# Performance work log

Measured on AMD Instinct MI355X. Metric: run time of the kernel, lower is better.

The kernel has to match this reference:

```python
import jax, jax.numpy as jnp
import numpy as np

N_NODES = 50000
N_EDGES = 800000
IN_C = 128
OUT_C = 128
BN_EPS = 1e-5


def setup_inputs() -> dict:
    key = jax.random.key(0)
    k1, k2, k3 = jax.random.split(key, 3)
    x = jax.random.normal(k1, (N_NODES, IN_C), dtype=jnp.float32)
    edge_index = jax.random.randint(k2, (2, N_EDGES), 0, N_NODES, dtype=jnp.int32)
    W = jax.random.normal(k3, (IN_C, OUT_C), dtype=jnp.float32) * (1.0 / np.sqrt(IN_C))
    bias = jnp.zeros((OUT_C,), dtype=jnp.float32)
    gamma = jnp.ones((OUT_C,), dtype=jnp.float32)
    beta = jnp.zeros((OUT_C,), dtype=jnp.float32)
    return {"x": x, "W": W, "bias": bias, "gamma": gamma, "beta": beta,
            "edge_index": edge_index}


def reference(x, W, bias, gamma, beta, edge_index):
    # GCNConv (PyG defaults): add self-loops, symmetric normalization, linear, scatter-add
    n = x.shape[0]
    h = x @ W  # [N, out_c]
    loops = jnp.arange(n, dtype=edge_index.dtype)
    row = jnp.concatenate([edge_index[0], loops])  # source nodes
    col = jnp.concatenate([edge_index[1], loops])  # target nodes
    # degree of targets (with self-loops, so deg >= 1)
    deg = jnp.zeros((n,), dtype=h.dtype).at[col].add(1.0)
    dinv = jax.lax.rsqrt(deg)
    norm = dinv[row] * dinv[col]  # [E+N]
    msg = h[row] * norm[:, None]  # gather + per-edge scale, [E+N, out_c]
    agg = jax.ops.segment_sum(msg, col, num_segments=n) + bias  # scatter-add
    # BatchNorm1d over node dimension (training-mode batch statistics)
    mean = jnp.mean(agg, axis=0)
    var = jnp.var(agg, axis=0)
    y = (agg - mean) * jax.lax.rsqrt(var + BN_EPS) * gamma + beta
    # ReLU; dropout is identity at inference
    return jax.nn.relu(y)
```

## Files before the change

kernel.cpp:

```cpp
#include <hip/hip_runtime.h>

#define N_NODES 50000
#define N_EDGES 800000
#define C 128
#define BN_EPS 1e-5f
#define BSHIFT 7
#define NBUCK ((N_NODES + 127) >> BSHIFT)
#define EPB 2048
#define A_BLOCKS ((N_EDGES + EPB - 1) / EPB)
#define EBUF 2560
#define GEMM_BLOCKS ((N_NODES + 63) / 64)
#define GATHER_BLOCKS 512
#define GATHER_WAVES (GATHER_BLOCKS * 8)

typedef __attribute__((ext_vector_type(8))) short bf16x8;
typedef __attribute__((ext_vector_type(4))) float f32x4;

__device__ __forceinline__ unsigned pack_bf16x2(float a, float b) {
    unsigned ua = __float_as_uint(a);
    ua = (ua + 0x7FFFu + ((ua >> 16) & 1u)) >> 16;
    unsigned ub = __float_as_uint(b);
    ub = (ub + 0x7FFFu + ((ub >> 16) & 1u)) >> 16;
    return ua | (ub << 16);
}

__device__ __forceinline__ unsigned short bf16_1(float a) {
    unsigned u = __float_as_uint(a);
    return (unsigned short)((u + 0x7FFFu + ((u >> 16) & 1u)) >> 16);
}

__device__ __forceinline__ float blo(unsigned u) { return __uint_as_float(u << 16); }
__device__ __forceinline__ float bhi(unsigned u) { return __uint_as_float(u & 0xFFFF0000u); }

__device__ __forceinline__ unsigned pack_f16x2(float a, float b) {
    _Float16 ha = (_Float16)a, hb = (_Float16)b;
    return (unsigned)__builtin_bit_cast(unsigned short, ha) |
           ((unsigned)__builtin_bit_cast(unsigned short, hb) << 16);
}
__device__ __forceinline__ float f16lo(unsigned u) {
    return (float)__builtin_bit_cast(_Float16, (unsigned short)(u & 0xFFFFu));
}
__device__ __forceinline__ float f16hi(unsigned u) {
    return (float)__builtin_bit_cast(_Float16, (unsigned short)(u >> 16));
}

__global__ void __launch_bounds__(256) k_scat(const int* __restrict__ row,
                                              const int* __restrict__ col,
                                              unsigned* __restrict__ bEdges,
                                              int* __restrict__ bOffsT,
                                              const float* __restrict__ W,
                                              unsigned* __restrict__ WTn,
                                              float* __restrict__ sums8) {
    int tid = threadIdx.x, w = blockIdx.x;
    if (w == A_BLOCKS) {
#pragma unroll
        for (int it = 0; it < 32; ++it) {
            int i = tid + (it << 8);
            int j = i & 3, l = (i >> 2) & 63, kt = (i >> 8) & 3, nt = i >> 10;
            int m = l & 15, q = l >> 4;
            int kr = kt * 32 + q * 8 + 2 * j;
            int n = nt * 16 + m;
            WTn[i] = pack_bf16x2(W[kr * C + n], W[(kr + 1) * C + n]);
        }
        for (int i = tid; i < 2048; i += 256) sums8[i] = 0.f;
        return;
    }
    __shared__ int hist[NBUCK];
    __shared__ int wsum[8];
    int lane = tid & 63, wid = tid >> 6;
    for (int i = tid; i < NBUCK; i += 256) hist[i] = 0;
    __syncthreads();
    int e0 = w * EPB;
    int nE = N_EDGES - e0; if (nE > EPB) nE = EPB;
    int myc[8], myr[8];
#pragma unroll
    for (int k = 0; k < 8; ++k) {
        int idx = tid + (k << 8);
        bool ok = idx < nE;
        myc[k] = ok ? col[e0 + idx] : -1;
        myr[k] = ok ? row[e0 + idx] : 0;
        if (ok) atomicAdd(&hist[myc[k] >> BSHIFT], 1);
    }
    __syncthreads();
    int v0 = hist[tid];
    int v1 = (tid + 256 < NBUCK) ? hist[tid + 256] : 0;
    int s0 = v0, s1 = v1;
#pragma unroll
    for (int d = 1; d < 64; d <<= 1) {
        int u0 = __shfl_up(s0, d, 64);
        int u1 = __shfl_up(s1, d, 64);
        if (lane >= d) { s0 += u0; s1 += u1; }
    }
    if (lane == 63) { wsum[wid] = s0; wsum[4 + wid] = s1; }
    __syncthreads();
    int tot0 = wsum[0] + wsum[1] + wsum[2] + wsum[3];
    int p0 = 0, p1 = tot0;
    for (int i = 0; i < wid; ++i) { p0 += wsum[i]; p1 += wsum[4 + i]; }
    int exc0 = p0 + s0 - v0;
    int exc1 = p1 + s1 - v1;
    bOffsT[tid * A_BLOCKS + w] = exc0;
    if (tid + 256 < NBUCK) bOffsT[(tid + 256) * A_BLOCKS + w] = exc1;
    if (tid == 0) bOffsT[NBUCK * A_BLOCKS + w] = nE;
    hist[tid] = exc0;
    if (tid + 256 < NBUCK) hist[tid + 256] = exc1;
    __syncthreads();
#pragma unroll
    for (int k = 0; k < 8; ++k) {
        if (myc[k] >= 0) {
            int b = myc[k] >> BSHIFT;
            int r = atomicAdd(&hist[b], 1);
            bEdges[(size_t)w * EPB + r] = (unsigned)myr[k] | ((unsigned)myc[k] << 16);
        }
    }
}

__global__ void __launch_bounds__(256) k_mid(const unsigned* __restrict__ bEdges,
                                             const int* __restrict__ bOffsT,
                                             int* __restrict__ offs,
                                             float* __restrict__ dinvArr,
                                             unsigned short* __restrict__ srcs,
                                             const float* __restrict__ x,
                                             const unsigned* __restrict__ WTn,
                                             unsigned short* __restrict__ g16) {
    __shared__ __align__(16) unsigned sm[4352];
    __shared__ int wsum[12];
    __shared__ int wtot;
    int tid = threadIdx.x;
    int lane = tid & 63, wid = tid >> 6;
    if (blockIdx.x < NBUCK) {
        const int b = blockIdx.x;
        int* sS = (int*)sm;
        int* sO = (int*)sm + 392;
        unsigned* ebuf = sm + 792;
        int* h = (int*)(sm + 792 + EBUF);
        int i1 = tid + 256;
        int st0 = bOffsT[b * A_BLOCKS + tid];
        int v0 = bOffsT[(b + 1) * A_BLOCKS + tid] - st0;
        int st1 = 0, v1 = 0;
        if (i1 < A_BLOCKS) {
            st1 = bOffsT[b * A_BLOCKS + i1];
            v1 = bOffsT[(b + 1) * A_BLOCKS + i1] - st1;
        }
        sS[tid] = st0;
        if (i1 < A_BLOCKS) sS[i1] = st1;
        if (tid < 128) h[tid] = 0;
        int ep = st0 + st1;
        int s0 = v0, s1 = v1;
#pragma unroll
        for (int d = 1; d < 64; d <<= 1) {
            int u0 = __shfl_up(s0, d, 64);
            int u1 = __shfl_up(s1, d, 64);
            if (lane >= d) { s0 += u0; s1 += u1; }
            ep += __shfl_xor(ep, d, 64);
        }
        if (lane == 63) { wsum[wid] = s0; wsum[4 + wid] = s1; }
        if (lane == 0) wsum[8 + wid] = ep;
        __syncthreads();
        int tot0 = wsum[0] + wsum[1] + wsum[2] + wsum[3];
        int tot1 = wsum[4] + wsum[5] + wsum[6] + wsum[7];
        int e0 = wsum[8] + wsum[9] + wsum[10] + wsum[11];
        int p0 = 0, p1 = tot0;
        for (int i = 0; i < wid; ++i) { p0 += wsum[i]; p1 += wsum[4 + i]; }
        sO[tid] = p0 + s0 - v0;
        if (i1 < A_BLOCKS) sO[i1] = p1 + s1 - v1;
        if (tid == 0) sO[A_BLOCKS] = tot0 + tot1;
        __syncthreads();
        int c = sO[A_BLOCKS];
        if (c > EBUF) c = EBUF;
        for (int seg = tid; seg < A_BLOCKS; seg += 256) {
            int o = sO[seg];
            int n = sO[seg + 1] - o;
            const unsigned* srcp = bEdges + (size_t)seg * EPB + sS[seg];
            for (int k = 0; k < n; ++k) {
                int dp = o + k;
                if (dp < EBUF) ebuf[dp] = srcp[k];
            }
        }
        __syncthreads();
        int n0 = b << BSHIFT;
        int nn = N_NODES - n0; if (nn > 128) nn = 128;
        for (int e = tid; e < c; e += 256)
            atomicAdd(&h[(int)(ebuf[e] >> 16) - n0], 1);
        __syncthreads();
        int v = 0, sc = 0;
        if (tid < 128) {
            int ln = tid & 63;
            v = h[tid];
            sc = v;
#pragma unroll
            for (int d = 1; d < 64; d <<= 1) {
                int u = __shfl_up(sc, d, 64);
                if (ln >= d) sc += u;
            }
            if (tid == 63) wtot = sc;
        }
        __syncthreads();
        if (tid < 128) {
            int ex = sc - v + ((tid >= 64) ? wtot : 0);
            if (tid < nn) {
                offs[n0 + tid] = e0 + ex;
                dinvArr[n0 + tid] = rsqrtf((float)v + 1.f);
            }
            h[tid] = ex;
        }
        __syncthreads();
        for (int e = tid; e < c; e += 256) {
            unsigned pe = ebuf[e];
            int r = atomicAdd(&h[(int)(pe >> 16) - n0], 1);
            srcs[e0 + r] = (unsigned short)(pe & 0xFFFFu);
        }
        if (b == NBUCK - 1 && tid == 0) offs[N_NODES] = N_EDGES;
    } else {
        unsigned* xs = sm;
        int r0 = (blockIdx.x - NBUCK) * 64;
        const float4* x4 = (const float4*)x;
#pragma unroll
        for (int it = 0; it < 8; ++it) {
            int i = tid + (it << 8);
            int r = i >> 5, c4 = i & 31;
            float4 v = {0.f, 0.f, 0.f, 0.f};
            if (r0 + r < N_NODES) v = x4[(size_t)(r0 + r) * 32 + c4];
            xs[r * 68 + c4 * 2]     = pack_bf16x2(v.x, v.y);
            xs[r * 68 + c4 * 2 + 1] = pack_bf16x2(v.z, v.w);
        }
        __syncthreads();
        int r0w = r0 + wid * 16;
        if (r0w >= N_NODES) return;
        int m = lane & 15, q = lane >> 4;
        bf16x8 afrag[4];
#pragma unroll
        for (int kt = 0; kt < 4; ++kt)
            afrag[kt] = *(const bf16x8*)&xs[(wid * 16 + m) * 68 + kt * 16 + q * 4];
        const uint4* B4 = (const uint4*)WTn;
        f32x4 acc[8];
#pragma unroll
        for (int nt = 0; nt < 8; ++nt)
            acc[nt][0] = acc[nt][1] = acc[nt][2] = acc[nt][3] = 0.f;
#pragma unroll
        for (int nt = 0; nt < 8; ++nt) {
#pragma unroll
            for (int kt = 0; kt < 4; ++kt) {
                uint4 braw = B4[(nt * 4 + kt) * 64 + lane];
                bf16x8 bfrag = __builtin_bit_cast(bf16x8, braw);
                acc[nt] = __builtin_amdgcn_mfma_f32_16x16x32_bf16(afrag[kt], bfrag, acc[nt], 0, 0, 0);
            }
        }
        int rb = r0w + q * 4;
#pragma unroll
        for (int nt = 0; nt < 8; ++nt) {
            int cbase = nt * 16 + m;
#pragma unroll
            for (int reg = 0; reg < 4; ++reg)
                g16[(size_t)(rb + reg) * C + cbase] = bf16_1(acc[nt][reg]);
        }
    }
}

#define ACC8S(v, d) { a[0]+=blo(v.x)*d; a[1]+=bhi(v.x)*d; a[2]+=blo(v.y)*d; a[3]+=bhi(v.y)*d; \
                      a[4]+=blo(v.z)*d; a[5]+=bhi(v.z)*d; a[6]+=blo(v.w)*d; a[7]+=bhi(v.w)*d; }
__global__ void __launch_bounds__(512) k_gather(const int* __restrict__ offs,
                                                const unsigned short* __restrict__ srcs,
                                                const uint4* __restrict__ g4,
                                                const float* __restrict__ dinvArr,
                                                unsigned* __restrict__ aggh,
                                                float* __restrict__ sums8) {
    __shared__ float lsA[8][32][4], lsQ[8][32][4];
    int tid = threadIdx.x;
    int lane = tid & 63, wid = tid >> 6;
    int l = lane & 15, q = lane >> 4;
    float sA[4] = {0.f, 0.f, 0.f, 0.f}, sQ[4] = {0.f, 0.f, 0.f, 0.f};
    int gw = blockIdx.x * 8 + wid;
    for (int node = gw; node < N_NODES; node += GATHER_WAVES) {
        int beg = offs[node], end = offs[node + 1];
        float dt = dinvArr[node];
        float a[8];
        if (q == 0) {
            uint4 u = g4[(size_t)node * 16 + l];
            a[0]=blo(u.x)*dt; a[1]=bhi(u.x)*dt; a[2]=blo(u.y)*dt; a[3]=bhi(u.y)*dt;
            a[4]=blo(u.z)*dt; a[5]=bhi(u.z)*dt; a[6]=blo(u.w)*dt; a[7]=bhi(u.w)*dt;
        } else {
#pragma unroll
            for (int i = 0; i < 8; ++i) a[i] = 0.f;
        }
        for (int base = beg; base < end; base += 64) {
            int nb = end - base; if (nb > 64) nb = 64;
            int sv = (base + lane < end) ? (int)srcs[base + lane] : 0;
            int j0 = 0;
            for (; j0 + 16 <= nb; j0 += 16) {
                int i0 = j0 + q;
                int s0 = __shfl(sv, i0, 64);
                int s1 = __shfl(sv, i0 + 4, 64);
                int s2 = __shfl(sv, i0 + 8, 64);
                int s3 = __shfl(sv, i0 + 12, 64);
                float d0 = dinvArr[s0], d1 = dinvArr[s1], d2 = dinvArr[s2], d3 = dinvArr[s3];
                uint4 v0 = g4[(size_t)s0 * 16 + l];
                uint4 v1 = g4[(size_t)s1 * 16 + l];
                uint4 v2 = g4[(size_t)s2 * 16 + l];
                uint4 v3 = g4[(size_t)s3 * 16 + l];
                ACC8S(v0, d0) ACC8S(v1, d1) ACC8S(v2, d2) ACC8S(v3, d3)
            }
            if (j0 < nb) {
#pragma unroll
                for (int k = 0; k < 4; ++k) {
                    int idx = j0 + q + 4 * k;
                    int s = __shfl(sv, idx, 64);
                    if (idx < nb) {
                        float dd = dinvArr[s];
                        uint4 v = g4[(size_t)s * 16 + l];
                        ACC8S(v, dd)
                    }
                }
            }
        }
#pragma unroll
        for (int i = 0; i < 8; ++i) {
            a[i] += __shfl_xor(a[i], 16, 64);
            a[i] += __shfl_xor(a[i], 32, 64);
        }
        if (q < 2) {
            float f0 = a[q * 4 + 0] * dt, f1 = a[q * 4 + 1] * dt;
            float f2 = a[q * 4 + 2] * dt, f3 = a[q * 4 + 3] * dt;
            sA[0] += f0; sQ[0] += f0 * f0;
            sA[1] += f1; sQ[1] += f1 * f1;
            sA[2] += f2; sQ[2] += f2 * f2;
            sA[3] += f3; sQ[3] += f3 * f3;
            uint2 pv; pv.x = pack_f16x2(f0, f1); pv.y = pack_f16x2(f2, f3);
            *(uint2*)(aggh + (size_t)node * 64 + l * 4 + q * 2) = pv;
        }
    }
    if (q < 2) {
#pragma unroll
        for (int i = 0; i < 4; ++i) {
            lsA[wid][l * 2 + q][i] = sA[i];
            lsQ[wid][l * 2 + q][i] = sQ[i];
        }
    }
    __syncthreads();
    if (tid < 128) {
        int ll = tid >> 3, qq = (tid >> 2) & 1, ii = tid & 3;
        float s = 0.f, sq = 0.f;
#pragma unroll
        for (int wd = 0; wd < 8; ++wd) {
            s  += lsA[wd][ll * 2 + qq][ii];
            sq += lsQ[wd][ll * 2 + qq][ii];
        }
        int slice = (blockIdx.x & 7) * 256;
        atomicAdd(&sums8[slice + tid], s);
        atomicAdd(&sums8[slice + 128 + tid], sq);
    }
}

__global__ void __launch_bounds__(256) k_final(const unsigned* __restrict__ aggh,
                                               float* __restrict__ out,
                                               const float* __restrict__ sums8,
                                               const float* __restrict__ gamma,
                                               const float* __restrict__ beta) {
    __shared__ float sc_s[C], sh_s[C];
    int tid = threadIdx.x;
    if (tid < C) {
        float s = 0.f, sq = 0.f;
#pragma unroll
        for (int k = 0; k < 8; ++k) {
            s  += sums8[k * 256 + tid];
            sq += sums8[k * 256 + 128 + tid];
        }
        float mean = s * (1.0f / N_NODES);
        float var = sq * (1.0f / N_NODES) - mean * mean;
        float sc = gamma[tid] * rsqrtf(var + BN_EPS);
        sc_s[tid] = sc;
        sh_s[tid] = beta[tid] - mean * sc;
    }
    __syncthreads();
    int i = blockIdx.x * 256 + tid;
    uint4 v = ((const uint4*)aggh)[i];
    int c = (i & 15) * 8;
    float4 o0, o1;
    o0.x = fmaxf(f16lo(v.x) * sc_s[c+0] + sh_s[c+0], 0.f);
    o0.y = fmaxf(f16hi(v.x) * sc_s[c+1] + sh_s[c+1], 0.f);
    o0.z = fmaxf(f16lo(v.y) * sc_s[c+2] + sh_s[c+2], 0.f);
    o0.w = fmaxf(f16hi(v.y) * sc_s[c+3] + sh_s[c+3], 0.f);
    o1.x = fmaxf(f16lo(v.z) * sc_s[c+4] + sh_s[c+4], 0.f);
    o1.y = fmaxf(f16hi(v.z) * sc_s[c+5] + sh_s[c+5], 0.f);
    o1.z = fmaxf(f16lo(v.w) * sc_s[c+6] + sh_s[c+6], 0.f);
    o1.w = fmaxf(f16hi(v.w) * sc_s[c+7] + sh_s[c+7], 0.f);
    float4* o = (float4*)(out + (size_t)i * 8);
    o[0] = o0; o[1] = o1;
}

extern "C" void kernel_launch(void* const* d_in, const int* in_sizes, int n_in,
                              void* d_out, int out_size, void* d_ws, size_t ws_size,
                              hipStream_t stream) {
    const float* x     = (const float*)d_in[0];
    const float* W     = (const float*)d_in[1];
    const float* gamma = (const float*)d_in[3];
    const float* beta  = (const float*)d_in[4];
    const int*   eidx  = (const int*)d_in[5];
    const int* row = eidx;
    const int* col = eidx + N_EDGES;

    float* out = (float*)d_out;

    unsigned* g      = (unsigned*)d_ws;
    unsigned* aggh   = g + (size_t)N_NODES * 64;
    unsigned* bEdges = aggh + (size_t)N_NODES * 64;
    unsigned* WTn    = bEdges + (size_t)A_BLOCKS * EPB;
    unsigned short* srcs = (unsigned short*)(WTn + 8192);
    int*   offs    = (int*)(srcs + N_EDGES);
    float* dinvArr = (float*)(offs + N_NODES + 4);
    float* sums8   = dinvArr + N_NODES;
    int*   bOffsT  = (int*)(sums8 + 2048);

    k_scat<<<A_BLOCKS + 1, 256, 0, stream>>>(row, col, bEdges, bOffsT, W, WTn, sums8);
    k_mid<<<NBUCK + GEMM_BLOCKS, 256, 0, stream>>>(bEdges, bOffsT, offs, dinvArr, srcs,
                                                   x, WTn, (unsigned short*)g);
    k_gather<<<GATHER_BLOCKS, 512, 0, stream>>>(offs, srcs, (const uint4*)g, dinvArr, aggh, sums8);
    k_final<<<N_NODES * 16 / 256, 256, 0, stream>>>(aggh, out, sums8, gamma, beta);
}
```

Before: 153.1 us.

## Software-pipeline node descriptors and neighbor indices in gather kernel

Replaces the CSR offset array with per-node (offset, degree) descriptors. The gather loop now prefetches the next node's neighbor indices and dinv values, plus the descriptor two nodes ahead, so their dependent loads overlap with the current node's feature gathers. dinv is loaded once per neighbor lane and broadcast with shuffles, and the target dinv is recomputed from the degree. This raises register pressure, which may lower occupancy.

```diff
diff --git a/kernel.cpp b/kernel.cpp
--- a/kernel.cpp
+++ b/kernel.cpp
@@ -116,7 +116,7 @@
 
 __global__ void __launch_bounds__(256) k_mid(const unsigned* __restrict__ bEdges,
                                              const int* __restrict__ bOffsT,
-                                             int* __restrict__ offs,
+                                             int2* __restrict__ nodeDesc,
                                              float* __restrict__ dinvArr,
                                              unsigned short* __restrict__ srcs,
                                              const float* __restrict__ x,
@@ -198,7 +198,7 @@
         if (tid < 128) {
             int ex = sc - v + ((tid >= 64) ? wtot : 0);
             if (tid < nn) {
-                offs[n0 + tid] = e0 + ex;
+                nodeDesc[n0 + tid] = make_int2(e0 + ex, v);
                 dinvArr[n0 + tid] = rsqrtf((float)v + 1.f);
             }
             h[tid] = ex;
@@ -209,7 +209,6 @@
             int r = atomicAdd(&h[(int)(pe >> 16) - n0], 1);
             srcs[e0 + r] = (unsigned short)(pe & 0xFFFFu);
         }
-        if (b == NBUCK - 1 && tid == 0) offs[N_NODES] = N_EDGES;
     } else {
         unsigned* xs = sm;
         int r0 = (blockIdx.x - NBUCK) * 64;
@@ -258,7 +257,38 @@
 
 #define ACC8S(v, d) { a[0]+=blo(v.x)*d; a[1]+=bhi(v.x)*d; a[2]+=blo(v.y)*d; a[3]+=bhi(v.y)*d; \
                       a[4]+=blo(v.z)*d; a[5]+=bhi(v.z)*d; a[6]+=blo(v.w)*d; a[7]+=bhi(v.w)*d; }
-__global__ void __launch_bounds__(512) k_gather(const int* __restrict__ offs,
+
+__device__ __forceinline__ void acc_batch(const uint4* __restrict__ g4, int l, int q,
+                                          int sv, float dvv, int nb, float* a) {
+    int j0 = 0;
+    for (; j0 + 16 <= nb; j0 += 16) {
+        int i0 = j0 + q;
+        int s0 = __shfl(sv, i0, 64);
+        int s1 = __shfl(sv, i0 + 4, 64);
+        int s2 = __shfl(sv, i0 + 8, 64);
+        int s3 = __shfl(sv, i0 + 12, 64);
+        float d0 = __shfl(dvv, i0, 64);
+        float d1 = __shfl(dvv, i0 + 4, 64);
+        float d2 = __shfl(dvv, i0 + 8, 64);
+        float d3 = __shfl(dvv, i0 + 12, 64);
+        uint4 v0 = g4[(size_t)s0 * 16 + l];
+        uint4 v1 = g4[(size_t)s1 * 16 + l];
+        uint4 v2 = g4[(size_t)s2 * 16 + l];
+        uint4 v3 = g4[(size_t)s3 * 16 + l];
+        ACC8S(v0, d0) ACC8S(v1, d1) ACC8S(v2, d2) ACC8S(v3, d3)
+    }
+    if (j0 < nb) {
+#pragma unroll
+        for (int k = 0; k < 4; ++k) {
+            int idx = j0 + q + 4 * k;
+            int s = __shfl(sv, idx, 64);
+            float d = __shfl(dvv, idx, 64);
+            if (idx < nb) { uint4 v = g4[(size_t)s * 16 + l]; ACC8S(v, d) }
+        }
+    }
+}
+
+__global__ void __launch_bounds__(512) k_gather(const int2* __restrict__ nodeDesc,
                                                 const unsigned short* __restrict__ srcs,
                                                 const uint4* __restrict__ g4,
                                                 const float* __restrict__ dinvArr,
@@ -270,47 +300,39 @@
     int l = lane & 15, q = lane >> 4;
     float sA[4] = {0.f, 0.f, 0.f, 0.f}, sQ[4] = {0.f, 0.f, 0.f, 0.f};
     int gw = blockIdx.x * 8 + wid;
-    for (int node = gw; node < N_NODES; node += GATHER_WAVES) {
-        int beg = offs[node], end = offs[node + 1];
-        float dt = dinvArr[node];
+
+    int nA = gw, nB = gw + GATHER_WAVES, nC = gw + 2 * GATHER_WAVES;
+    int2 dA = {0, 0}, dB = {0, 0};
+    int svA = 0; float dvA = 0.f;
+    if (nA < N_NODES) {
+        dA = nodeDesc[nA];
+        if (lane < dA.y) { svA = srcs[dA.x + lane]; dvA = dinvArr[svA]; }
+    }
+    if (nB < N_NODES) dB = nodeDesc[nB];
+
+    while (nA < N_NODES) {
+        int svB = 0; float dvB = 0.f;
+        if (nB < N_NODES && lane < dB.y) { svB = srcs[dB.x + lane]; dvB = dinvArr[svB]; }
+        int2 dC = {0, 0};
+        if (nC < N_NODES) dC = nodeDesc[nC];
+
+        float dt = rsqrtf((float)dA.y + 1.f);
         float a[8];
         if (q == 0) {
-            uint4 u = g4[(size_t)node * 16 + l];
+            uint4 u = g4[(size_t)nA * 16 + l];
             a[0]=blo(u.x)*dt; a[1]=bhi(u.x)*dt; a[2]=blo(u.y)*dt; a[3]=bhi(u.y)*dt;
             a[4]=blo(u.z)*dt; a[5]=bhi(u.z)*dt; a[6]=blo(u.w)*dt; a[7]=bhi(u.w)*dt;
         } else {
 #pragma unroll
             for (int i = 0; i < 8; ++i) a[i] = 0.f;
         }
-        for (int base = beg; base < end; base += 64) {
-            int nb = end - base; if (nb > 64) nb = 64;
-            int sv = (base + lane < end) ? (int)srcs[base + lane] : 0;
-            int j0 = 0;
-            for (; j0 + 16 <= nb; j0 += 16) {
-                int i0 = j0 + q;
-                int s0 = __shfl(sv, i0, 64);
-                int s1 = __shfl(sv, i0 + 4, 64);
-                int s2 = __shfl(sv, i0 + 8, 64);
-                int s3 = __shfl(sv, i0 + 12, 64);
-                float d0 = dinvArr[s0], d1 = dinvArr[s1], d2 = dinvArr[s2], d3 = dinvArr[s3];
-                uint4 v0 = g4[(size_t)s0 * 16 + l];
-                uint4 v1 = g4[(size_t)s1 * 16 + l];
-                uint4 v2 = g4[(size_t)s2 * 16 + l];
-                uint4 v3 = g4[(size_t)s3 * 16 + l];
-                ACC8S(v0, d0) ACC8S(v1, d1) ACC8S(v2, d2) ACC8S(v3, d3)
-            }
-            if (j0 < nb) {
-#pragma unroll
-                for (int k = 0; k < 4; ++k) {
-                    int idx = j0 + q + 4 * k;
-                    int s = __shfl(sv, idx, 64);
-                    if (idx < nb) {
-                        float dd = dinvArr[s];
-                        uint4 v = g4[(size_t)s * 16 + l];
-                        ACC8S(v, dd)
-                    }
-                }
-            }
+        int nb0 = dA.y < 64 ? dA.y : 64;
+        acc_batch(g4, l, q, svA, dvA, nb0, a);
+        for (int base = dA.x + 64; base < dA.x + dA.y; base += 64) {
+            int nb = dA.x + dA.y - base; if (nb > 64) nb = 64;
+            int sv2 = 0; float dv2 = 0.f;
+            if (lane < nb) { sv2 = srcs[base + lane]; dv2 = dinvArr[sv2]; }
+            acc_batch(g4, l, q, sv2, dv2, nb, a);
         }
 #pragma unroll
         for (int i = 0; i < 8; ++i) {
@@ -325,9 +347,12 @@
             sA[2] += f2; sQ[2] += f2 * f2;
             sA[3] += f3; sQ[3] += f3 * f3;
             uint2 pv; pv.x = pack_f16x2(f0, f1); pv.y = pack_f16x2(f2, f3);
-            *(uint2*)(aggh + (size_t)node * 64 + l * 4 + q * 2) = pv;
-        }
-    }
+            *(uint2*)(aggh + (size_t)nA * 64 + l * 4 + q * 2) = pv;
+        }
+        nA = nB; dA = dB; svA = svB; dvA = dvB;
+        nB = nC; dB = dC; nC += GATHER_WAVES;
+    }
+
     if (q < 2) {
 #pragma unroll
         for (int i = 0; i < 4; ++i) {
@@ -405,14 +430,14 @@
     unsigned* bEdges = aggh + (size_t)N_NODES * 64;
     unsigned* WTn    = bEdges + (size_t)A_BLOCKS * EPB;
     unsigned short* srcs = (unsigned short*)(WTn + 8192);
-    int*   offs    = (int*)(srcs + N_EDGES);
-    float* dinvArr = (float*)(offs + N_NODES + 4);
-    float* sums8   = dinvArr + N_NODES;
-    int*   bOffsT  = (int*)(sums8 + 2048);
+    int2*  nodeDesc = (int2*)(srcs + N_EDGES);
+    float* dinvArr  = (float*)(nodeDesc + N_NODES);
+    float* sums8    = dinvArr + N_NODES;
+    int*   bOffsT   = (int*)(sums8 + 2048);
 
     k_scat<<<A_BLOCKS + 1, 256, 0, stream>>>(row, col, bEdges, bOffsT, W, WTn, sums8);
-    k_mid<<<NBUCK + GEMM_BLOCKS, 256, 0, stream>>>(bEdges, bOffsT, offs, dinvArr, srcs,
+    k_mid<<<NBUCK + GEMM_BLOCKS, 256, 0, stream>>>(bEdges, bOffsT, nodeDesc, dinvArr, srcs,
                                                    x, WTn, (unsigned short*)g);
-    k_gather<<<GATHER_BLOCKS, 512, 0, stream>>>(offs, srcs, (const uint4*)g, dinvArr, aggh, sums8);
+    k_gather<<<GATHER_BLOCKS, 512, 0, stream>>>(nodeDesc, srcs, (const uint4*)g, dinvArr, aggh, sums8);
     k_final<<<N_NODES * 16 / 256, 256, 0, stream>>>(aggh, out, sums8, gamma, beta);
 }
```

Measured after the change: 155.9 us. About the same (+1.8%).
